# Kernel tuning notes

Hardware: AMD Instinct MI355X
Metric: run time of the kernel (lower is better)

Reference implementation:

```python
import jax, jax.numpy as jnp
import numpy as np

B, T, D = 8, 2048, 512


def setup_inputs() -> dict:
    key = jax.random.key(0)
    ks = jax.random.split(key, 12)
    s = 1.0 / np.sqrt(D)
    return {
        "x": jax.random.normal(ks[0], (B, T, D), dtype=jnp.float32),
        "Wq": jax.random.normal(ks[1], (D, D), dtype=jnp.float32) * s,
        "bq": jax.random.normal(ks[2], (D,), dtype=jnp.float32) * 0.01,
        "Wk": jax.random.normal(ks[3], (D, D), dtype=jnp.float32) * s,
        "bk": jax.random.normal(ks[4], (D,), dtype=jnp.float32) * 0.01,
        "Wv": jax.random.normal(ks[5], (D, D), dtype=jnp.float32) * s,
        "bv": jax.random.normal(ks[6], (D,), dtype=jnp.float32) * 0.01,
        "Wbeta": jax.random.normal(ks[7], (1, D), dtype=jnp.float32) * s,
        "bbeta": jax.random.normal(ks[8], (1,), dtype=jnp.float32) * 0.01,
        "Wo": jax.random.normal(ks[9], (D, D), dtype=jnp.float32) * s,
        "bo": jax.random.normal(ks[10], (D,), dtype=jnp.float32) * 0.01,
    }


def _l2_normalize(v, eps=1e-12):
    # torch F.normalize(p=2, dim=-1): v / max(||v||, eps)
    n = jnp.sqrt(jnp.sum(v * v, axis=-1, keepdims=True))
    return v / jnp.maximum(n, eps)


def _deltanet(x, Wq, bq, Wk, bk, Wv, bv, Wbeta, bbeta, Wo, bo):
    Q = x @ Wq.T + bq                      # [B,T,D]
    K = _l2_normalize(x @ Wk.T + bk)       # [B,T,D], unit-norm keys
    V = x @ Wv.T + bv                      # [B,T,D]
    Beta = jax.nn.sigmoid(K @ Wbeta.T + bbeta)  # [B,T,1]

    # time-major for scan: [T,B,D] / [T,B,1]
    Qt = jnp.swapaxes(Q, 0, 1)
    Kt = jnp.swapaxes(K, 0, 1)
    Vt = jnp.swapaxes(V, 0, 1)
    Bt = jnp.swapaxes(Beta, 0, 1)

    S0 = jnp.zeros((x.shape[0], x.shape[-1], x.shape[-1]), dtype=x.dtype)

    def step(S, inp):
        q, k, v, beta = inp                 # [B,D],[B,D],[B,D],[B,1]
        Sk = jnp.einsum("bij,bj->bi", S, k)           # S k_t
        b = beta[:, :, None]                            # [B,1,1]
        # S_t = S - beta (S k) k^T + beta v k^T
        S = S - b * (Sk[:, :, None] * k[:, None, :]) + b * (v[:, :, None] * k[:, None, :])
        o = jnp.einsum("bij,bj->bi", S, q)              # o_t = S_t q_t
        return S, o

    _, Ot = jax.lax.scan(step, S0, (Qt, Kt, Vt, Bt))    # [T,B,D]
    O = jnp.swapaxes(Ot, 0, 1)                          # [B,T,D]
    return O @ Wo.T + bo


def reference(x, Wq, bq, Wk, bk, Wv, bv, Wbeta, bbeta, Wo, bo):
    return _deltanet(x, Wq, bq, Wk, bk, Wv, bv, Wbeta, bbeta, Wo, bo)
```

## Files before the change

### kernel.cpp

```cpp
#include <hip/hip_runtime.h>

#define D 512
#define T 2048
#define BATCH 8
#define M_ROWS (BATCH*T)
#define CHK 64
#define NCHB 32
#define NCHUNK 256

typedef __attribute__((ext_vector_type(8))) short short8;
typedef __attribute__((ext_vector_type(4))) float floatx4;

__device__ __forceinline__ unsigned short f2bf(float f) {
  unsigned int u = __float_as_uint(f);
  u += 0x7FFFu + ((u >> 16) & 1u);
  return (unsigned short)(u >> 16);
}
__device__ __forceinline__ float bf2f(unsigned int h) {
  return __uint_as_float(h << 16);
}
__device__ __forceinline__ float wave_allreduce(float v) {
  #pragma unroll
  for (int m = 32; m; m >>= 1) v += __shfl_xor(v, m, 64);
  return v;
}
__device__ __forceinline__ void unpack8(uint4 r, float f[8]) {
  f[0] = bf2f(r.x & 0xffffu); f[1] = bf2f(r.x >> 16);
  f[2] = bf2f(r.y & 0xffffu); f[3] = bf2f(r.y >> 16);
  f[4] = bf2f(r.z & 0xffffu); f[5] = bf2f(r.z >> 16);
  f[6] = bf2f(r.w & 0xffffu); f[7] = bf2f(r.w >> 16);
}

__global__ __launch_bounds__(256) void cast_kernel(const float* __restrict__ src,
                                                   unsigned short* __restrict__ dst, int n) {
  int idx = (blockIdx.x * 256 + threadIdx.x) * 8;
  if (idx >= n) return;
  const float4* sp = (const float4*)(src + idx);
  float4 a = sp[0], b = sp[1];
  uint4 o;
  o.x = f2bf(a.x) | ((unsigned)f2bf(a.y) << 16);
  o.y = f2bf(a.z) | ((unsigned)f2bf(a.w) << 16);
  o.z = f2bf(b.x) | ((unsigned)f2bf(b.y) << 16);
  o.w = f2bf(b.z) | ((unsigned)f2bf(b.w) << 16);
  *(uint4*)(dst + idx) = o;
}

#define BM 128
#define BN 128
#define BK 32

template<bool OUT_BF16>
__global__ __launch_bounds__(256) void gemm_nt(
    const unsigned short* __restrict__ A, const unsigned short* __restrict__ Bw,
    const float* __restrict__ bias, void* __restrict__ Cout, int M, int N, int K)
{
  __shared__ __align__(16) unsigned short As[BM * BK];
  __shared__ __align__(16) unsigned short Bs[BN * BK];
  int tid  = threadIdx.x;
  int lane = tid & 63;
  int wave = tid >> 6;
  int waveM = (wave >> 1) * 64;
  int waveN = (wave & 1) * 64;
  int lrow = lane & 15;
  int quad = lane >> 4;

  floatx4 acc[4][4];
  #pragma unroll
  for (int a_ = 0; a_ < 4; ++a_)
    #pragma unroll
    for (int b_ = 0; b_ < 4; ++b_) acc[a_][b_] = (floatx4){0.f, 0.f, 0.f, 0.f};

  const unsigned short* Ap = A  + (size_t)(blockIdx.y * BM) * K;
  const unsigned short* Bp = Bw + (size_t)(blockIdx.x * BN) * K;
  int r0 = tid >> 2;
  int c0 = (tid & 3) * 8;

  for (int k0 = 0; k0 < K; k0 += BK) {
    __syncthreads();
    *(uint4*)&As[r0 * BK + c0]        = *(const uint4*)&Ap[(size_t)r0 * K + k0 + c0];
    *(uint4*)&As[(r0 + 64) * BK + c0] = *(const uint4*)&Ap[(size_t)(r0 + 64) * K + k0 + c0];
    *(uint4*)&Bs[r0 * BK + c0]        = *(const uint4*)&Bp[(size_t)r0 * K + k0 + c0];
    *(uint4*)&Bs[(r0 + 64) * BK + c0] = *(const uint4*)&Bp[(size_t)(r0 + 64) * K + k0 + c0];
    __syncthreads();
    short8 af[4], bf[4];
    #pragma unroll
    for (int mt = 0; mt < 4; ++mt)
      af[mt] = *(const short8*)&As[(waveM + mt * 16 + lrow) * BK + quad * 8];
    #pragma unroll
    for (int nt = 0; nt < 4; ++nt)
      bf[nt] = *(const short8*)&Bs[(waveN + nt * 16 + lrow) * BK + quad * 8];
    #pragma unroll
    for (int mt = 0; mt < 4; ++mt)
      #pragma unroll
      for (int nt = 0; nt < 4; ++nt)
        acc[mt][nt] = __builtin_amdgcn_mfma_f32_16x16x32_bf16(af[mt], bf[nt], acc[mt][nt], 0, 0, 0);
  }

  int cm = blockIdx.y * BM + waveM;
  int cn = blockIdx.x * BN + waveN;
  #pragma unroll
  for (int nt = 0; nt < 4; ++nt) {
    int col = cn + nt * 16 + lrow;
    float bv = bias[col];
    #pragma unroll
    for (int mt = 0; mt < 4; ++mt) {
      #pragma unroll
      for (int r = 0; r < 4; ++r) {
        int row = cm + mt * 16 + quad * 4 + r;
        float v = acc[mt][nt][r] + bv;
        if (OUT_BF16) ((unsigned short*)Cout)[(size_t)row * N + col] = f2bf(v);
        else          ((float*)Cout)[(size_t)row * N + col] = v;
      }
    }
  }
}

__global__ __launch_bounds__(256) void norm_beta_kernel(
    unsigned short* __restrict__ Kb, const float* __restrict__ Wbeta,
    const float* __restrict__ bbeta, float* __restrict__ Beta)
{
  int w = blockIdx.x * 4 + (threadIdx.x >> 6);
  int lane = threadIdx.x & 63;
  unsigned short* kp = Kb + (size_t)w * D + lane * 8;
  uint4 raw = *(uint4*)kp;
  float kv[8]; unpack8(raw, kv);
  float ss = 0.f;
  #pragma unroll
  for (int m = 0; m < 8; ++m) ss += kv[m] * kv[m];
  ss = wave_allreduce(ss);
  float inv = 1.0f / fmaxf(sqrtf(ss), 1e-12f);
  const float* wb = Wbeta + lane * 8;
  float dotp = 0.f;
  #pragma unroll
  for (int m = 0; m < 8; ++m) { kv[m] *= inv; dotp += kv[m] * wb[m]; }
  uint4 o;
  o.x = f2bf(kv[0]) | ((unsigned)f2bf(kv[1]) << 16);
  o.y = f2bf(kv[2]) | ((unsigned)f2bf(kv[3]) << 16);
  o.z = f2bf(kv[4]) | ((unsigned)f2bf(kv[5]) << 16);
  o.w = f2bf(kv[6]) | ((unsigned)f2bf(kv[7]) << 16);
  *(uint4*)kp = o;
  dotp = wave_allreduce(dotp);
  if (lane == 0) Beta[w] = 1.0f / (1.0f + expf(-(dotp + bbeta[0])));
}

__global__ __launch_bounds__(256) void transpose_kv(
    const unsigned short* __restrict__ Kb, const unsigned short* __restrict__ Vb,
    unsigned short* __restrict__ KT, unsigned short* __restrict__ VT)
{
  int cb = blockIdx.x & 255;
  const unsigned short* src = (blockIdx.x < 256 ? Kb : Vb) + (size_t)cb * 64 * 512;
  unsigned short* dst = (blockIdx.x < 256 ? KT : VT) + (size_t)cb * 32768;
  int lane = threadIdx.x & 63, w = threadIdx.x >> 6;
  int lr = lane & 15, quad = lane >> 4;
  short8 a0, a1;
  #pragma unroll
  for (int j = 0; j < 8; ++j) {
    a0[j] = (quad == (lr >> 3)     && j == (lr & 7)) ? (short)0x3F80 : (short)0;
    a1[j] = (quad == 2 + (lr >> 3) && j == (lr & 7)) ? (short)0x3F80 : (short)0;
  }
  int t0 = w * 16;
  #pragma unroll 4
  for (int dk0 = 0; dk0 < 16; ++dk0) {
    short8 b = *(const short8*)&src[(size_t)(t0 + lr) * 512 + dk0 * 32 + quad * 8];
    floatx4 z = (floatx4){0.f,0.f,0.f,0.f};
    floatx4 c0 = __builtin_amdgcn_mfma_f32_16x16x32_bf16(a0, b, z, 0, 0, 0);
    floatx4 c1 = __builtin_amdgcn_mfma_f32_16x16x32_bf16(a1, b, z, 0, 0, 0);
    #pragma unroll
    for (int r = 0; r < 4; ++r) {
      dst[(dk0 * 32 +      quad * 4 + r) * 64 + t0 + lr] = f2bf(c0[r]);
      dst[(dk0 * 32 + 16 + quad * 4 + r) * 64 + t0 + lr] = f2bf(c1[r]);
    }
  }
}

__global__ __launch_bounds__(256) void gram_kernel(
    const unsigned short* __restrict__ Qb, const unsigned short* __restrict__ Kb,
    const float* __restrict__ Beta, float* __restrict__ Abuf,
    unsigned short* __restrict__ Msb)
{
  int cb = blockIdx.x, tid = threadIdx.x, lane = tid & 63, w = tid >> 6;
  int lr = lane & 15, quad = lane >> 4;
  const unsigned short* kc = Kb + (size_t)cb * 64 * 512;
  const unsigned short* qc = Qb + (size_t)cb * 64 * 512;
  floatx4 accK[4], accQ[4];
  #pragma unroll
  for (int nt = 0; nt < 4; ++nt) { accK[nt] = (floatx4){0,0,0,0}; accQ[nt] = (floatx4){0,0,0,0}; }
  short8 ak = *(const short8*)&kc[(w * 16 + lr) * 512 + quad * 8];
  short8 aq = *(const short8*)&qc[(w * 16 + lr) * 512 + quad * 8];
  short8 bk[4];
  #pragma unroll
  for (int nt = 0; nt < 4; ++nt)
    bk[nt] = *(const short8*)&kc[(nt * 16 + lr) * 512 + quad * 8];
  #pragma unroll
  for (int ks = 0; ks < 16; ++ks) {
    short8 akn, aqn, bkn[4];
    if (ks < 15) {
      int off = (ks + 1) * 32 + quad * 8;
      akn = *(const short8*)&kc[(w * 16 + lr) * 512 + off];
      aqn = *(const short8*)&qc[(w * 16 + lr) * 512 + off];
      #pragma unroll
      for (int nt = 0; nt < 4; ++nt)
        bkn[nt] = *(const short8*)&kc[(nt * 16 + lr) * 512 + off];
    }
    #pragma unroll
    for (int nt = 0; nt < 4; ++nt) {
      accK[nt] = __builtin_amdgcn_mfma_f32_16x16x32_bf16(ak, bk[nt], accK[nt], 0, 0, 0);
      accQ[nt] = __builtin_amdgcn_mfma_f32_16x16x32_bf16(aq, bk[nt], accQ[nt], 0, 0, 0);
    }
    if (ks < 15) {
      ak = akn; aq = aqn;
      #pragma unroll
      for (int nt = 0; nt < 4; ++nt) bk[nt] = bkn[nt];
    }
  }
  #pragma unroll
  for (int nt = 0; nt < 4; ++nt)
    #pragma unroll
    for (int r = 0; r < 4; ++r) {
      int t = w * 16 + quad * 4 + r;
      int j = nt * 16 + lr;
      float bt = Beta[cb * 64 + t];
      Abuf[(size_t)cb * 4096 + t * 64 + j] = (j < t) ? bt * accK[nt][r] : 0.f;
      Msb[(size_t)cb * 4096 + t * 64 + j]  = f2bf((j <= t) ? accQ[nt][r] : 0.f);
    }
}

__global__ __launch_bounds__(64) void tinv_kernel(
    const float* __restrict__ Abuf, const float* __restrict__ Beta,
    unsigned short* __restrict__ Tib)
{
  __shared__ float XT[64 * 68];
  int lane = threadIdx.x;
  int cb = blockIdx.x;
  float bl = Beta[cb * 64 + lane];
  const float* Ab = Abuf + (size_t)cb * 4096;
  unsigned short* To = Tib + (size_t)cb * 4096;
  float* Xr = XT + lane * 68;
  #pragma unroll
  for (int j = 0; j < 68; j += 4) *(float4*)&Xr[j] = (float4){0.f,0.f,0.f,0.f};
  for (int t = 0; t < 64; ++t) {
    const float* Ar = Ab + t * 64;
    float p0 = 0.f, p1 = 0.f, p2 = 0.f, p3 = 0.f;
    for (int jb = 0; jb < t; jb += 4) {
      float4 xv = *(const float4*)&Xr[jb];
      float4 av = *(const float4*)&Ar[jb];
      p0 = fmaf(av.x, xv.x, p0); p1 = fmaf(av.y, xv.y, p1);
      p2 = fmaf(av.z, xv.z, p2); p3 = fmaf(av.w, xv.w, p3);
    }
    float y = ((lane == t) ? 1.f : 0.f) - (p0 + p1) - (p2 + p3);
    Xr[t] = y;
    To[t * 64 + lane] = f2bf(y * bl);
  }
}

__global__ __launch_bounds__(256) void wu_kernel(
    const unsigned short* __restrict__ Tib, const unsigned short* __restrict__ KT,
    const unsigned short* __restrict__ VT, unsigned short* __restrict__ Wneg,
    unsigned short* __restrict__ Ubar)
{
  __shared__ __align__(16) unsigned short WL[64 * 512];
  __shared__ __align__(16) unsigned short UL[64 * 512];
  int cb = blockIdx.x, tid = threadIdx.x, lane = tid & 63, w = tid >> 6;
  int lr = lane & 15, quad = lane >> 4;
  short8 af0 = *(const short8*)&Tib[(size_t)cb * 4096 + (w * 16 + lr) * 64 + quad * 8];
  short8 af1 = *(const short8*)&Tib[(size_t)cb * 4096 + (w * 16 + lr) * 64 + 32 + quad * 8];
  const unsigned short* ktc = KT + (size_t)cb * 32768 + lr * 64 + quad * 8;
  const unsigned short* vtc = VT + (size_t)cb * 32768 + lr * 64 + quad * 8;
  int tbase = w * 16 + quad * 4;
  #pragma unroll 4
  for (int nt = 0; nt < 32; ++nt) {
    short8 bk0 = *(const short8*)(ktc + nt * 1024);
    short8 bk1 = *(const short8*)(ktc + nt * 1024 + 32);
    short8 bv0 = *(const short8*)(vtc + nt * 1024);
    short8 bv1 = *(const short8*)(vtc + nt * 1024 + 32);
    floatx4 z = (floatx4){0.f,0.f,0.f,0.f};
    floatx4 aw = __builtin_amdgcn_mfma_f32_16x16x32_bf16(af0, bk0, z, 0, 0, 0);
    aw = __builtin_amdgcn_mfma_f32_16x16x32_bf16(af1, bk1, aw, 0, 0, 0);
    floatx4 au = __builtin_amdgcn_mfma_f32_16x16x32_bf16(af0, bv0, z, 0, 0, 0);
    au = __builtin_amdgcn_mfma_f32_16x16x32_bf16(af1, bv1, au, 0, 0, 0);
    int bi = nt * 2 + (lr >> 3);
    int lo = lr & 7;
    #pragma unroll
    for (int r = 0; r < 4; ++r) {
      int tt = tbase + r;
      int bis = bi ^ (tt & 7);
      WL[tt * 512 + bis * 8 + lo] = f2bf(-aw[r]);
      UL[tt * 512 + bis * 8 + lo] = f2bf(au[r]);
    }
  }
  __syncthreads();
  unsigned short* wd = Wneg + (size_t)cb * 32768;
  unsigned short* ud = Ubar + (size_t)cb * 32768;
  #pragma unroll
  for (int it = 0; it < 16; ++it) {
    int e = it * 2048 + tid * 8;
    int row = e >> 9, col = e & 511;
    int bis = (col >> 3) ^ (row & 7);
    *(uint4*)&wd[e] = *(const uint4*)&WL[row * 512 + bis * 8];
    *(uint4*)&ud[e] = *(const uint4*)&UL[row * 512 + bis * 8];
  }
}

__global__ __launch_bounds__(1024) void seq_kernel(
    const unsigned short* __restrict__ Wneg, const unsigned short* __restrict__ Qb,
    const unsigned short* __restrict__ Ubar, const unsigned short* __restrict__ Msb,
    const unsigned short* __restrict__ KT, unsigned short* __restrict__ Ob)
{
  __shared__ __align__(16) unsigned short Sb[16 * 520];
  __shared__ __align__(16) float DUp[64 * 64];
  __shared__ __align__(16) float DOp[64 * 64];
  __shared__ __align__(16) unsigned short Ut[16 * 72];
  int blk = blockIdx.x;
  int b = blk >> 5, vs = blk & 31;
  int vg0 = vs * 16;
  int tid = threadIdx.x, lane = tid & 63, wave = tid >> 6;
  int lr = lane & 15, quad = lane >> 4;
  int kg = wave & 3;
  int tm = wave >> 2;
  int ct = tid >> 4, cv = tid & 15;

  floatx4 sacc[2];
  sacc[0] = (floatx4){0.f,0.f,0.f,0.f};
  sacc[1] = (floatx4){0.f,0.f,0.f,0.f};

  int cb0 = b * NCHB;
  for (int ch = 0; ch < NCHB; ++ch) {
    int cb = cb0 + ch;
    size_t tokb = (size_t)cb * 64;
    short8 wnf[4], qff[4];
    {
      const unsigned short* wr = Wneg + (tokb + tm * 16 + lr) * 512 + kg * 128 + quad * 8;
      const unsigned short* qr = Qb   + (tokb + tm * 16 + lr) * 512 + kg * 128 + quad * 8;
      #pragma unroll
      for (int ks = 0; ks < 4; ++ks) {
        wnf[ks] = *(const short8*)(wr + ks * 32);
        qff[ks] = *(const short8*)(qr + ks * 32);
      }
    }
    unsigned short ubv = Ubar[(tokb + ct) * 512 + vg0 + cv];
    short8 ktf[2][2];
    {
      const unsigned short* kr = KT + (size_t)cb * 32768 + (wave * 32 + lr) * 64 + quad * 8;
      ktf[0][0] = *(const short8*)(kr);
      ktf[0][1] = *(const short8*)(kr + 32);
      ktf[1][0] = *(const short8*)(kr + 16 * 64);
      ktf[1][1] = *(const short8*)(kr + 16 * 64 + 32);
    }
    short8 msf0, msf1;
    if (kg == 0) {
      const unsigned short* mr = Msb + (size_t)cb * 4096 + (tm * 16 + lr) * 64 + quad * 8;
      msf0 = *(const short8*)(mr);
      msf1 = *(const short8*)(mr + 32);
    }
    #pragma unroll
    for (int s = 0; s < 2; ++s)
      #pragma unroll
      for (int r = 0; r < 4; ++r)
        Sb[(quad * 4 + r) * 520 + wave * 32 + s * 16 + lr] = f2bf(sacc[s][r]);
    __syncthreads();
    floatx4 du = (floatx4){0.f,0.f,0.f,0.f};
    floatx4 dq = (floatx4){0.f,0.f,0.f,0.f};
    #pragma unroll
    for (int ks = 0; ks < 4; ++ks) {
      short8 sb = *(const short8*)&Sb[lr * 520 + kg * 128 + ks * 32 + quad * 8];
      du = __builtin_amdgcn_mfma_f32_16x16x32_bf16(wnf[ks], sb, du, 0, 0, 0);
      dq = __builtin_amdgcn_mfma_f32_16x16x32_bf16(qff[ks], sb, dq, 0, 0, 0);
    }
    #pragma unroll
    for (int r = 0; r < 4; ++r) {
      int t = tm * 16 + quad * 4 + r;
      DUp[t * 64 + lr * 4 + kg] = du[r];
      DOp[t * 64 + lr * 4 + kg] = dq[r];
    }
    __syncthreads();
    {
      float4 p = *(const float4*)&DUp[ct * 64 + cv * 4];
      float uval = (p.x + p.y) + (p.z + p.w) + bf2f(ubv);
      Ut[cv * 72 + ct] = f2bf(uval);
    }
    __syncthreads();
    short8 a20 = *(const short8*)&Ut[lr * 72 + quad * 8];
    short8 a21 = *(const short8*)&Ut[lr * 72 + 32 + quad * 8];
    #pragma unroll
    for (int s = 0; s < 2; ++s) {
      sacc[s] = __builtin_amdgcn_mfma_f32_16x16x32_bf16(a20, ktf[s][0], sacc[s], 0, 0, 0);
      sacc[s] = __builtin_amdgcn_mfma_f32_16x16x32_bf16(a21, ktf[s][1], sacc[s], 0, 0, 0);
    }
    if (kg == 0) {
      floatx4 oo;
      #pragma unroll
      for (int r = 0; r < 4; ++r) {
        int t = tm * 16 + quad * 4 + r;
        float4 p = *(const float4*)&DOp[t * 64 + lr * 4];
        oo[r] = (p.x + p.y) + (p.z + p.w);
      }
      oo = __builtin_amdgcn_mfma_f32_16x16x32_bf16(msf0, a20, oo, 0, 0, 0);
      oo = __builtin_amdgcn_mfma_f32_16x16x32_bf16(msf1, a21, oo, 0, 0, 0);
      unsigned short* ob = Ob + (tokb + tm * 16 + quad * 4) * 512 + vg0 + lr;
      #pragma unroll
      for (int r = 0; r < 4; ++r) ob[(size_t)r * 512] = f2bf(oo[r]);
    }
  }
}

extern "C" void kernel_launch(void* const* d_in, const int* in_sizes, int n_in,
                              void* d_out, int out_size, void* d_ws, size_t ws_size,
                              hipStream_t stream) {
  const float* x     = (const float*)d_in[0];
  const float* Wq    = (const float*)d_in[1];
  const float* bq    = (const float*)d_in[2];
  const float* Wk    = (const float*)d_in[3];
  const float* bk    = (const float*)d_in[4];
  const float* Wv    = (const float*)d_in[5];
  const float* bv    = (const float*)d_in[6];
  const float* Wbeta = (const float*)d_in[7];
  const float* bbeta = (const float*)d_in[8];
  const float* Wo    = (const float*)d_in[9];
  const float* bo    = (const float*)d_in[10];

  const size_t NE = (size_t)M_ROWS * D;
  const size_t DD = (size_t)D * D;
  unsigned short* Qb  = (unsigned short*)d_ws;
  unsigned short* Kb  = Qb + NE;
  unsigned short* Vb  = Kb + NE;
  unsigned short* Xb  = Vb + NE;
  unsigned short* Wqb = Xb + NE;
  unsigned short* Wkb = Wqb + DD;
  unsigned short* Wvb = Wkb + DD;
  unsigned short* Wob = Wvb + DD;
  float* Beta = (float*)(Wob + DD);
  unsigned short* KT  = (unsigned short*)(Beta + M_ROWS);
  float* Abuf = (float*)(KT + NE);
  unsigned short* Msb = (unsigned short*)(Abuf + (size_t)NCHUNK * 4096);
  unsigned short* Tib = Msb + (size_t)NCHUNK * 4096;
  unsigned short* VT  = Tib + (size_t)NCHUNK * 4096;

  cast_kernel<<<(int)(NE / 2048), 256, 0, stream>>>(x, Xb, (int)NE);
  cast_kernel<<<(int)(DD / 2048), 256, 0, stream>>>(Wq, Wqb, (int)DD);
  cast_kernel<<<(int)(DD / 2048), 256, 0, stream>>>(Wk, Wkb, (int)DD);
  cast_kernel<<<(int)(DD / 2048), 256, 0, stream>>>(Wv, Wvb, (int)DD);
  cast_kernel<<<(int)(DD / 2048), 256, 0, stream>>>(Wo, Wob, (int)DD);

  dim3 gg(D / BN, M_ROWS / BM);
  gemm_nt<true><<<gg, 256, 0, stream>>>(Xb, Wqb, bq, Qb, M_ROWS, D, D);
  gemm_nt<true><<<gg, 256, 0, stream>>>(Xb, Wkb, bk, Kb, M_ROWS, D, D);
  gemm_nt<true><<<gg, 256, 0, stream>>>(Xb, Wvb, bv, Vb, M_ROWS, D, D);

  norm_beta_kernel<<<M_ROWS / 4, 256, 0, stream>>>(Kb, Wbeta, bbeta, Beta);

  transpose_kv<<<2 * NCHUNK, 256, 0, stream>>>(Kb, Vb, KT, VT);
  gram_kernel<<<NCHUNK, 256, 0, stream>>>(Qb, Kb, Beta, Abuf, Msb);
  tinv_kernel<<<NCHUNK, 64, 0, stream>>>(Abuf, Beta, Tib);
  wu_kernel<<<NCHUNK, 256, 0, stream>>>(Tib, KT, VT, Xb, Kb);

  seq_kernel<<<NCHUNK, 1024, 0, stream>>>(Xb, Qb, Kb, Msb, KT, Vb);

  gemm_nt<false><<<gg, 256, 0, stream>>>(Vb, Wob, bo, (float*)d_out, M_ROWS, D, D);
}
```

Baseline: 487.7 us.

## Split gram and wu kernels across two blocks per chunk, repad seq partial sums

The gram and wu kernels now launch two blocks per chunk, each covering half the rows/columns or half the feature dimension, so 512 blocks fill the GPU instead of 256. The wu kernel halves its LDS tiles, which should allow more blocks per CU. The seq kernel's reduction buffers change to a per-key-group layout padded to stride 17 to cut LDS bank conflicts, at the cost of scalar reads in place of float4 loads. The seq kernel's block-to-batch mapping is also interleaved so that neighbouring blocks handle different batches.

```diff
diff --git a/kernel.cpp b/kernel.cpp
--- a/kernel.cpp
+++ b/kernel.cpp
@@ -178,47 +178,49 @@
     const float* __restrict__ Beta, float* __restrict__ Abuf,
     unsigned short* __restrict__ Msb)
 {
-  int cb = blockIdx.x, tid = threadIdx.x, lane = tid & 63, w = tid >> 6;
+  int cb = blockIdx.x >> 1, half = blockIdx.x & 1;
+  int tid = threadIdx.x, lane = tid & 63, w = tid >> 6;
   int lr = lane & 15, quad = lane >> 4;
+  int trow = half * 32 + (w & 1) * 16;
+  int ctb  = (w >> 1) * 32;
   const unsigned short* kc = Kb + (size_t)cb * 64 * 512;
   const unsigned short* qc = Qb + (size_t)cb * 64 * 512;
-  floatx4 accK[4], accQ[4];
-  #pragma unroll
-  for (int nt = 0; nt < 4; ++nt) { accK[nt] = (floatx4){0,0,0,0}; accQ[nt] = (floatx4){0,0,0,0}; }
-  short8 ak = *(const short8*)&kc[(w * 16 + lr) * 512 + quad * 8];
-  short8 aq = *(const short8*)&qc[(w * 16 + lr) * 512 + quad * 8];
-  short8 bk[4];
-  #pragma unroll
-  for (int nt = 0; nt < 4; ++nt)
-    bk[nt] = *(const short8*)&kc[(nt * 16 + lr) * 512 + quad * 8];
+  floatx4 accK[2], accQ[2];
+  #pragma unroll
+  for (int nt = 0; nt < 2; ++nt) { accK[nt] = (floatx4){0,0,0,0}; accQ[nt] = (floatx4){0,0,0,0}; }
+  short8 ak = *(const short8*)&kc[(trow + lr) * 512 + quad * 8];
+  short8 aq = *(const short8*)&qc[(trow + lr) * 512 + quad * 8];
+  short8 bk[2];
+  #pragma unroll
+  for (int nt = 0; nt < 2; ++nt)
+    bk[nt] = *(const short8*)&kc[(ctb + nt * 16 + lr) * 512 + quad * 8];
   #pragma unroll
   for (int ks = 0; ks < 16; ++ks) {
-    short8 akn, aqn, bkn[4];
+    short8 akn, aqn, bkn[2];
     if (ks < 15) {
       int off = (ks + 1) * 32 + quad * 8;
-      akn = *(const short8*)&kc[(w * 16 + lr) * 512 + off];
-      aqn = *(const short8*)&qc[(w * 16 + lr) * 512 + off];
-      #pragma unroll
-      for (int nt = 0; nt < 4; ++nt)
-        bkn[nt] = *(const short8*)&kc[(nt * 16 + lr) * 512 + off];
-    }
-    #pragma unroll
-    for (int nt = 0; nt < 4; ++nt) {
+      akn = *(const short8*)&kc[(trow + lr) * 512 + off];
+      aqn = *(const short8*)&qc[(trow + lr) * 512 + off];
+      #pragma unroll
+      for (int nt = 0; nt < 2; ++nt)
+        bkn[nt] = *(const short8*)&kc[(ctb + nt * 16 + lr) * 512 + off];
+    }
+    #pragma unroll
+    for (int nt = 0; nt < 2; ++nt) {
       accK[nt] = __builtin_amdgcn_mfma_f32_16x16x32_bf16(ak, bk[nt], accK[nt], 0, 0, 0);
       accQ[nt] = __builtin_amdgcn_mfma_f32_16x16x32_bf16(aq, bk[nt], accQ[nt], 0, 0, 0);
     }
     if (ks < 15) {
       ak = akn; aq = aqn;
-      #pragma unroll
-      for (int nt = 0; nt < 4; ++nt) bk[nt] = bkn[nt];
-    }
-  }
-  #pragma unroll
-  for (int nt = 0; nt < 4; ++nt)
+      bk[0] = bkn[0]; bk[1] = bkn[1];
+    }
+  }
+  #pragma unroll
+  for (int nt = 0; nt < 2; ++nt)
     #pragma unroll
     for (int r = 0; r < 4; ++r) {
-      int t = w * 16 + quad * 4 + r;
-      int j = nt * 16 + lr;
+      int t = trow + quad * 4 + r;
+      int j = ctb + nt * 16 + lr;
       float bt = Beta[cb * 64 + t];
       Abuf[(size_t)cb * 4096 + t * 64 + j] = (j < t) ? bt * accK[nt][r] : 0.f;
       Msb[(size_t)cb * 4096 + t * 64 + j]  = f2bf((j <= t) ? accQ[nt][r] : 0.f);
@@ -258,17 +260,18 @@
     const unsigned short* __restrict__ VT, unsigned short* __restrict__ Wneg,
     unsigned short* __restrict__ Ubar)
 {
-  __shared__ __align__(16) unsigned short WL[64 * 512];
-  __shared__ __align__(16) unsigned short UL[64 * 512];
-  int cb = blockIdx.x, tid = threadIdx.x, lane = tid & 63, w = tid >> 6;
+  __shared__ __align__(16) unsigned short WL[64 * 256];
+  __shared__ __align__(16) unsigned short UL[64 * 256];
+  int cb = blockIdx.x >> 1, dh = blockIdx.x & 1;
+  int tid = threadIdx.x, lane = tid & 63, w = tid >> 6;
   int lr = lane & 15, quad = lane >> 4;
   short8 af0 = *(const short8*)&Tib[(size_t)cb * 4096 + (w * 16 + lr) * 64 + quad * 8];
   short8 af1 = *(const short8*)&Tib[(size_t)cb * 4096 + (w * 16 + lr) * 64 + 32 + quad * 8];
-  const unsigned short* ktc = KT + (size_t)cb * 32768 + lr * 64 + quad * 8;
-  const unsigned short* vtc = VT + (size_t)cb * 32768 + lr * 64 + quad * 8;
+  const unsigned short* ktc = KT + (size_t)cb * 32768 + (size_t)dh * 16384 + lr * 64 + quad * 8;
+  const unsigned short* vtc = VT + (size_t)cb * 32768 + (size_t)dh * 16384 + lr * 64 + quad * 8;
   int tbase = w * 16 + quad * 4;
   #pragma unroll 4
-  for (int nt = 0; nt < 32; ++nt) {
+  for (int nt = 0; nt < 16; ++nt) {
     short8 bk0 = *(const short8*)(ktc + nt * 1024);
     short8 bk1 = *(const short8*)(ktc + nt * 1024 + 32);
     short8 bv0 = *(const short8*)(vtc + nt * 1024);
@@ -284,20 +287,20 @@
     for (int r = 0; r < 4; ++r) {
       int tt = tbase + r;
       int bis = bi ^ (tt & 7);
-      WL[tt * 512 + bis * 8 + lo] = f2bf(-aw[r]);
-      UL[tt * 512 + bis * 8 + lo] = f2bf(au[r]);
+      WL[tt * 256 + bis * 8 + lo] = f2bf(-aw[r]);
+      UL[tt * 256 + bis * 8 + lo] = f2bf(au[r]);
     }
   }
   __syncthreads();
-  unsigned short* wd = Wneg + (size_t)cb * 32768;
-  unsigned short* ud = Ubar + (size_t)cb * 32768;
-  #pragma unroll
-  for (int it = 0; it < 16; ++it) {
+  unsigned short* wd = Wneg + (size_t)cb * 32768 + dh * 256;
+  unsigned short* ud = Ubar + (size_t)cb * 32768 + dh * 256;
+  #pragma unroll
+  for (int it = 0; it < 8; ++it) {
     int e = it * 2048 + tid * 8;
-    int row = e >> 9, col = e & 511;
+    int row = e >> 8, col = e & 255;
     int bis = (col >> 3) ^ (row & 7);
-    *(uint4*)&wd[e] = *(const uint4*)&WL[row * 512 + bis * 8];
-    *(uint4*)&ud[e] = *(const uint4*)&UL[row * 512 + bis * 8];
+    *(uint4*)&wd[row * 512 + col] = *(const uint4*)&WL[row * 256 + bis * 8];
+    *(uint4*)&ud[row * 512 + col] = *(const uint4*)&UL[row * 256 + bis * 8];
   }
 }
 
@@ -307,11 +310,11 @@
     const unsigned short* __restrict__ KT, unsigned short* __restrict__ Ob)
 {
   __shared__ __align__(16) unsigned short Sb[16 * 520];
-  __shared__ __align__(16) float DUp[64 * 64];
-  __shared__ __align__(16) float DOp[64 * 64];
+  __shared__ __align__(16) float DUp[4 * 1088];
+  __shared__ __align__(16) float DOp[4 * 1088];
   __shared__ __align__(16) unsigned short Ut[16 * 72];
   int blk = blockIdx.x;
-  int b = blk >> 5, vs = blk & 31;
+  int b = blk & 7, vs = blk >> 3;
   int vg0 = vs * 16;
   int tid = threadIdx.x, lane = tid & 63, wave = tid >> 6;
   int lr = lane & 15, quad = lane >> 4;
@@ -369,13 +372,13 @@
     #pragma unroll
     for (int r = 0; r < 4; ++r) {
       int t = tm * 16 + quad * 4 + r;
-      DUp[t * 64 + lr * 4 + kg] = du[r];
-      DOp[t * 64 + lr * 4 + kg] = dq[r];
+      DUp[kg * 1088 + t * 17 + lr] = du[r];
+      DOp[kg * 1088 + t * 17 + lr] = dq[r];
     }
     __syncthreads();
     {
-      float4 p = *(const float4*)&DUp[ct * 64 + cv * 4];
-      float uval = (p.x + p.y) + (p.z + p.w) + bf2f(ubv);
+      int o = ct * 17 + cv;
+      float uval = (DUp[o] + DUp[1088 + o]) + (DUp[2176 + o] + DUp[3264 + o]) + bf2f(ubv);
       Ut[cv * 72 + ct] = f2bf(uval);
     }
     __syncthreads();
@@ -390,9 +393,8 @@
       floatx4 oo;
       #pragma unroll
       for (int r = 0; r < 4; ++r) {
-        int t = tm * 16 + quad * 4 + r;
-        float4 p = *(const float4*)&DOp[t * 64 + lr * 4];
-        oo[r] = (p.x + p.y) + (p.z + p.w);
+        int o = (tm * 16 + quad * 4 + r) * 17 + lr;
+        oo[r] = (DOp[o] + DOp[1088 + o]) + (DOp[2176 + o] + DOp[3264 + o]);
       }
       oo = __builtin_amdgcn_mfma_f32_16x16x32_bf16(msf0, a20, oo, 0, 0, 0);
       oo = __builtin_amdgcn_mfma_f32_16x16x32_bf16(msf1, a21, oo, 0, 0, 0);
@@ -449,9 +451,9 @@
   norm_beta_kernel<<<M_ROWS / 4, 256, 0, stream>>>(Kb, Wbeta, bbeta, Beta);
 
   transpose_kv<<<2 * NCHUNK, 256, 0, stream>>>(Kb, Vb, KT, VT);
-  gram_kernel<<<NCHUNK, 256, 0, stream>>>(Qb, Kb, Beta, Abuf, Msb);
+  gram_kernel<<<2 * NCHUNK, 256, 0, stream>>>(Qb, Kb, Beta, Abuf, Msb);
   tinv_kernel<<<NCHUNK, 64, 0, stream>>>(Abuf, Beta, Tib);
-  wu_kernel<<<NCHUNK, 256, 0, stream>>>(Tib, KT, VT, Xb, Kb);
+  wu_kernel<<<2 * NCHUNK, 256, 0, stream>>>(Tib, KT, VT, Xb, Kb);
 
   seq_kernel<<<NCHUNK, 1024, 0, stream>>>(Xb, Qb, Kb, Msb, KT, Vb);
 
```

Result: no change. 488.9 us (+0.3%).
